# Kernel tuning notes

Hardware: AMD Instinct MI355X
Metric: run time of the kernel (lower is better)

## Reference

```python
import jax, jax.numpy as jnp
import numpy as np

N_PEGS = 32      # 33 holes, one empty at start
N_ACTIONS = 132  # 33 positions * 4 moves


def _constants():
    # English peg-solitaire board: 7x7 cross, 33 holes; hole 0 is the center (3,3).
    moves = np.array([[-1, 0], [1, 0], [0, -1], [0, 1]], dtype=np.int64)
    cells = [(i, j) for i in range(7) for j in range(7) if (2 <= i <= 4) or (2 <= j <= 4)]
    cells.remove((3, 3))
    grid = np.array([(3, 3)] + cells, dtype=np.int64)          # (33, 2)
    p2i = {tuple(p): k for k, p in enumerate(grid)}
    pos_ids = np.repeat(np.arange(33), 4)                      # (132,)
    move_ids = np.tile(np.arange(4), 33)                       # (132,)
    apos = grid[pos_ids]                                       # (132, 2)
    amov = moves[move_ids]
    midp = apos + amov
    tgtp = apos + 2 * amov
    mid_idx = np.array([p2i.get(tuple(p), 0) for p in midp], dtype=np.int64)
    tgt_idx = np.array([p2i.get(tuple(p), 0) for p in tgtp], dtype=np.int64)
    oob = np.array([(tuple(m) not in p2i) or (tuple(t) not in p2i)
                    for m, t in zip(midp, tgtp)], dtype=bool)  # (132,)
    return dict(
        action_pos_ids=jnp.asarray(pos_ids, dtype=jnp.int32),
        action_mid_indices=jnp.asarray(mid_idx, dtype=jnp.int32),
        action_target_indices=jnp.asarray(tgt_idx, dtype=jnp.int32),
        oob_mask=jnp.asarray(oob),
        i_indices=jnp.asarray(grid[:, 0], dtype=jnp.int32),
        j_indices=jnp.asarray(grid[:, 1], dtype=jnp.int32),
    )


def setup_inputs() -> dict:
    key = jax.random.key(0)
    n = 262144
    k1, k2, k3, k4 = jax.random.split(key, 4)
    pegs = (jax.random.uniform(k1, (n, 33)) > 0.5).astype(jnp.float32)
    n_pegs = jax.random.randint(k2, (n,), 2, 32).astype(jnp.int32)
    done = jnp.zeros((n,), dtype=bool)
    total_reward = jax.random.uniform(k3, (n,), dtype=jnp.float32)
    actions = jax.random.randint(k4, (n,), 0, N_ACTIONS).astype(jnp.int32)
    inp = {"pegs": pegs, "n_pegs": n_pegs, "done": done,
           "total_reward": total_reward, "actions": actions}
    inp.update(_constants())
    return inp


def _feasible(pegs, done, action_pos_ids, action_mid_indices,
              action_target_indices, oob_mask):
    # (n, 132) boolean feasible-action mask
    mask = ~oob_mask[None, :]
    no_peg = pegs == 0.0
    mask = mask & ~no_peg[:, action_pos_ids]          # source must have a peg
    mask = mask & (pegs[:, action_mid_indices] > 0)   # mid must have a peg
    mask = mask & (pegs[:, action_target_indices] == 0)  # target must be empty
    return mask & ~done[:, None]


def reference(pegs, n_pegs, done, total_reward, actions,
              action_pos_ids, action_mid_indices, action_target_indices,
              oob_mask, i_indices, j_indices):
    n = pegs.shape[0]
    env = jnp.arange(n)
    pos = action_pos_ids[actions]
    mid = action_mid_indices[actions]
    tgt = action_target_indices[actions]
    # execute the jump (same write order as torch: pos<-0, mid<-0, target<-1)
    pegs = pegs.at[env, pos].set(0.0).at[env, mid].set(0.0).at[env, tgt].set(1.0)
    n_pegs = n_pegs - 1
    rewards = jnp.where(n_pegs == 1, 1.0, 1.0 / (N_PEGS - 1)).astype(jnp.float32)
    done_win = n_pegs == 1
    feasible = _feasible(pegs, done, action_pos_ids, action_mid_indices,
                         action_target_indices, oob_mask)
    done_new = done_win | ~feasible.any(axis=1)
    total_reward = total_reward + rewards
    # state: (n, 7, 7, 3)
    ch0 = jnp.zeros((n, 7, 7), dtype=pegs.dtype).at[:, i_indices, j_indices].set(pegs)
    npf = n_pegs.astype(jnp.float32)
    peg_ratio = (npf - 1.0) / (N_PEGS - 1)
    removed_ratio = (N_PEGS - npf) / (N_PEGS - 1)
    states = jnp.stack([
        ch0,
        jnp.broadcast_to(peg_ratio[:, None, None], (n, 7, 7)),
        jnp.broadcast_to(removed_ratio[:, None, None], (n, 7, 7)),
    ], axis=-1)
    return rewards, states, done_new, pegs, n_pegs, total_reward
```

## Files before the change

### kernel.cpp

```cpp
#include <hip/hip_runtime.h>


#define NTH 256
#define WPB 4
#define EPW 64

typedef float f32x4 __attribute__((ext_vector_type(4)));

__device__ constexpr int C2B[33] = {
    24,  2,  3,  4,  9, 10, 11, 14, 15, 16, 17, 18, 19, 20,
    21, 22, 23, 25, 26, 27, 28, 29, 30, 31, 32, 33, 34,
    37, 38, 39, 44, 45, 46};

constexpr unsigned long long cross_mask() {
    unsigned long long b = 0;
    for (int i = 0; i < 7; ++i)
        for (int j = 0; j < 7; ++j)
            if ((i >= 2 && i <= 4) || (j >= 2 && j <= 4))
                b |= 1ull << (i * 7 + j);
    return b;
}
constexpr unsigned long long cols_le(int jmax) {
    unsigned long long b = 0;
    for (int i = 0; i < 7; ++i)
        for (int j = 0; j <= jmax; ++j) b |= 1ull << (i * 7 + j);
    return b;
}
constexpr unsigned long long cols_ge(int jmin) {
    unsigned long long b = 0;
    for (int i = 0; i < 7; ++i)
        for (int j = jmin; j < 7; ++j) b |= 1ull << (i * 7 + j);
    return b;
}
constexpr unsigned long long B_MASK = cross_mask();
constexpr unsigned long long C_LE4  = cols_le(4);
constexpr unsigned long long C_GE2  = cols_ge(2);

__device__ __forceinline__ void wave_lds_fence() {
    asm volatile("s_waitcnt lgkmcnt(0)" ::: "memory");
    __builtin_amdgcn_sched_barrier(0);
}

__global__ __launch_bounds__(NTH) void peg_step(
    const float* __restrict__ pegs_in,
    const int* __restrict__ n_pegs_in,
    const unsigned char* __restrict__ done_in,
    const float* __restrict__ tot_rew_in,
    const int* __restrict__ actions,
    const int* __restrict__ pos_ids,
    const int* __restrict__ mid_idx,
    const int* __restrict__ tgt_idx,
    const int* __restrict__ i_ind,
    const int* __restrict__ j_ind,
    float* __restrict__ out,
    int n)
{
    __shared__ __align__(16) float s_pegs[WPB][EPW * 33];
    __shared__ unsigned long long s_bb[WPB][EPW];
    __shared__ float s_r1[WPB][EPW], s_r2[WPB][EPW];

    const int t    = threadIdx.x;
    const int w    = t >> 6;
    const int lane = t & 63;
    const int ew0  = blockIdx.x * (WPB * EPW) + w * EPW;
    const int e    = ew0 + lane;

    {
        const f32x4* src = (const f32x4*)(pegs_in + (size_t)ew0 * 33);
        f32x4* dst = (f32x4*)s_pegs[w];
        #pragma unroll
        for (int i = lane; i < EPW * 33 / 4; i += 64) dst[i] = src[i];
    }

    const int a         = actions[e];
    const int np_new    = n_pegs_in[e] - 1;
    const bool done_old = (done_in[e] != 0);
    const float tot     = tot_rew_in[e];
    const int p = pos_ids[a], m = mid_idx[a], g = tgt_idx[a];
    const int bp = i_ind[p] * 7 + j_ind[p];
    const int bm = i_ind[m] * 7 + j_ind[m];
    const int bg = i_ind[g] * 7 + j_ind[g];

    const float rw  = (np_new == 1) ? 1.0f : (1.0f / 31.0f);
    const float npf = (float)np_new;
    out[e]                   = rw;
    out[(size_t)182 * n + e] = npf;
    out[(size_t)183 * n + e] = tot + rw;

    wave_lds_fence();

    float* row = s_pegs[w] + lane * 33;
    unsigned long long P = 0;
    #pragma unroll
    for (int c = 0; c < 33; ++c)
        P |= (unsigned long long)(row[c] != 0.0f) << C2B[c];

    row[p] = 0.0f;
    row[m] = 0.0f;
    row[g] = 1.0f;
    P &= ~(1ull << bp);
    P &= ~(1ull << bm);
    P |=  (1ull << bg);

    const unsigned long long E = ~P & B_MASK;
    const unsigned long long feas =
        (P & (P >> 1) & (E >> 2)  & C_LE4) |
        (P & (P << 1) & (E << 2)  & C_GE2) |
        (P & (P >> 7) & (E >> 14))         |
        (P & (P << 7) & (E << 14));

    const bool dn = (np_new == 1) | done_old | (feas == 0ull);
    out[(size_t)148 * n + e] = dn ? 1.0f : 0.0f;

    s_bb[w][lane] = P;
    s_r1[w][lane] = (npf - 1.0f)  * (1.0f / 31.0f);
    s_r2[w][lane] = (32.0f - npf) * (1.0f / 31.0f);

    wave_lds_fence();

    {
        const f32x4* src = (const f32x4*)s_pegs[w];
        f32x4* dst = (f32x4*)(out + (size_t)149 * n + (size_t)ew0 * 33);
        #pragma unroll
        for (int i = lane; i < EPW * 33 / 4; i += 64) dst[i] = src[i];
    }

    {
        f32x4* dst = (f32x4*)(out + (size_t)n + (size_t)ew0 * 147);
        const int total = EPW * 147 / 4;
        for (int q = lane; q < total; q += 64) {
            const int f4 = q * 4;
            int env = f4 / 147;
            int el  = f4 - env * 147;
            unsigned long long bb = s_bb[w][env];
            float r1 = s_r1[w][env], r2 = s_r2[w][env];
            f32x4 v;
            #pragma unroll
            for (int r = 0; r < 4; ++r) {
                if (el == 147) {
                    el = 0; ++env;
                    bb = s_bb[w][env]; r1 = s_r1[w][env]; r2 = s_r2[w][env];
                }
                const int rc = el / 3;
                const int ch = el - rc * 3;
                v[r] = (ch == 0) ? (float)((unsigned int)(bb >> rc) & 1u)
                                 : ((ch == 1) ? r1 : r2);
                ++el;
            }
            dst[q] = v;
        }
    }
}

extern "C" void kernel_launch(void* const* d_in, const int* in_sizes, int n_in,
                              void* d_out, int out_size, void* d_ws, size_t ws_size,
                              hipStream_t stream) {
    const float* pegs          = (const float*)d_in[0];
    const int* n_pegs          = (const int*)d_in[1];
    const unsigned char* done  = (const unsigned char*)d_in[2];
    const float* total_reward  = (const float*)d_in[3];
    const int* actions         = (const int*)d_in[4];
    const int* pos_ids         = (const int*)d_in[5];
    const int* mid_idx         = (const int*)d_in[6];
    const int* tgt_idx         = (const int*)d_in[7];
    const int* i_ind           = (const int*)d_in[9];
    const int* j_ind           = (const int*)d_in[10];
    float* out = (float*)d_out;

    int n = in_sizes[1];
    dim3 grid(n / (WPB * EPW)), block(NTH);
    hipLaunchKernelGGL(peg_step, grid, block, 0, stream,
                       pegs, n_pegs, done, total_reward, actions,
                       pos_ids, mid_idx, tgt_idx, i_ind, j_ind, out, n);
}
```

Before: 44.66 us.

## Pack peg rows into LDS bitmasks instead of staging float rows

New measurement: 44.83 us. About the same (+0.4%).

```diff
diff --git a/kernel.cpp b/kernel.cpp
--- a/kernel.cpp
+++ b/kernel.cpp
@@ -11,6 +11,8 @@
     24,  2,  3,  4,  9, 10, 11, 14, 15, 16, 17, 18, 19, 20,
     21, 22, 23, 25, 26, 27, 28, 29, 30, 31, 32, 33, 34,
     37, 38, 39, 44, 45, 46};
+
+constexpr unsigned long long MASK33 = (1ull << 33) - 1;
 
 constexpr unsigned long long cross_mask() {
     unsigned long long b = 0;
@@ -41,7 +43,7 @@
     __builtin_amdgcn_sched_barrier(0);
 }
 
-__global__ __launch_bounds__(NTH) void peg_step(
+__global__ __launch_bounds__(NTH, 6) void peg_step(
     const float* __restrict__ pegs_in,
     const int* __restrict__ n_pegs_in,
     const unsigned char* __restrict__ done_in,
@@ -50,12 +52,10 @@
     const int* __restrict__ pos_ids,
     const int* __restrict__ mid_idx,
     const int* __restrict__ tgt_idx,
-    const int* __restrict__ i_ind,
-    const int* __restrict__ j_ind,
     float* __restrict__ out,
     int n)
 {
-    __shared__ __align__(16) float s_pegs[WPB][EPW * 33];
+    __shared__ unsigned long long s_cm[WPB][EPW + 1];
     __shared__ unsigned long long s_bb[WPB][EPW];
     __shared__ float s_r1[WPB][EPW], s_r2[WPB][EPW];
 
@@ -65,21 +65,19 @@
     const int ew0  = blockIdx.x * (WPB * EPW) + w * EPW;
     const int e    = ew0 + lane;
 
-    {
-        const f32x4* src = (const f32x4*)(pegs_in + (size_t)ew0 * 33);
-        f32x4* dst = (f32x4*)s_pegs[w];
-        #pragma unroll
-        for (int i = lane; i < EPW * 33 / 4; i += 64) dst[i] = src[i];
-    }
+    s_cm[w][lane] = 0ull;
+
+    const f32x4* src = (const f32x4*)(pegs_in + (size_t)ew0 * 33);
+    f32x4 r[8], r8;
+    #pragma unroll
+    for (int k = 0; k < 8; ++k) r[k] = src[lane + 64 * k];
+    if (lane < 16) r8 = src[512 + lane];
 
     const int a         = actions[e];
     const int np_new    = n_pegs_in[e] - 1;
     const bool done_old = (done_in[e] != 0);
     const float tot     = tot_rew_in[e];
     const int p = pos_ids[a], m = mid_idx[a], g = tgt_idx[a];
-    const int bp = i_ind[p] * 7 + j_ind[p];
-    const int bm = i_ind[m] * 7 + j_ind[m];
-    const int bg = i_ind[g] * 7 + j_ind[g];
 
     const float rw  = (np_new == 1) ? 1.0f : (1.0f / 31.0f);
     const float npf = (float)np_new;
@@ -87,20 +85,46 @@
     out[(size_t)182 * n + e] = npf;
     out[(size_t)183 * n + e] = tot + rw;
 
+    {
+        unsigned long long* cm = s_cm[w];
+        #pragma unroll
+        for (int k = 0; k < 8; ++k) {
+            const int q   = lane + 64 * k;
+            const int f   = q * 4;
+            const int env = f / 33;
+            const int c   = f - env * 33;
+            const unsigned mm = (r[k][0] != 0.0f) | ((r[k][1] != 0.0f) << 1) |
+                                ((r[k][2] != 0.0f) << 2) | ((r[k][3] != 0.0f) << 3);
+            const unsigned long long full = (unsigned long long)mm << c;
+            atomicOr(&cm[env], full & MASK33);
+            const unsigned long long hi = full >> 33;
+            if (hi) atomicOr(&cm[env + 1], hi);
+        }
+        if (lane < 16) {
+            const int q   = 512 + lane;
+            const int f   = q * 4;
+            const int env = f / 33;
+            const int c   = f - env * 33;
+            const unsigned mm = (r8[0] != 0.0f) | ((r8[1] != 0.0f) << 1) |
+                                ((r8[2] != 0.0f) << 2) | ((r8[3] != 0.0f) << 3);
+            const unsigned long long full = (unsigned long long)mm << c;
+            atomicOr(&cm[env], full & MASK33);
+            const unsigned long long hi = full >> 33;
+            if (hi) atomicOr(&cm[env + 1], hi);
+        }
+    }
+
     wave_lds_fence();
 
-    float* row = s_pegs[w] + lane * 33;
+    unsigned long long cm = s_cm[w][lane];
+    cm &= ~(1ull << p);
+    cm &= ~(1ull << m);
+    cm |=  (1ull << g);
+
     unsigned long long P = 0;
     #pragma unroll
     for (int c = 0; c < 33; ++c)
-        P |= (unsigned long long)(row[c] != 0.0f) << C2B[c];
-
-    row[p] = 0.0f;
-    row[m] = 0.0f;
-    row[g] = 1.0f;
-    P &= ~(1ull << bp);
-    P &= ~(1ull << bm);
-    P |=  (1ull << bg);
+        P |= ((cm >> c) & 1ull) << C2B[c];
 
     const unsigned long long E = ~P & B_MASK;
     const unsigned long long feas =
@@ -112,6 +136,7 @@
     const bool dn = (np_new == 1) | done_old | (feas == 0ull);
     out[(size_t)148 * n + e] = dn ? 1.0f : 0.0f;
 
+    s_cm[w][lane] = cm;
     s_bb[w][lane] = P;
     s_r1[w][lane] = (npf - 1.0f)  * (1.0f / 31.0f);
     s_r2[w][lane] = (32.0f - npf) * (1.0f / 31.0f);
@@ -119,10 +144,23 @@
     wave_lds_fence();
 
     {
-        const f32x4* src = (const f32x4*)s_pegs[w];
         f32x4* dst = (f32x4*)(out + (size_t)149 * n + (size_t)ew0 * 33);
         #pragma unroll
-        for (int i = lane; i < EPW * 33 / 4; i += 64) dst[i] = src[i];
+        for (int k = 0; k < 9; ++k) {
+            const int q = lane + 64 * k;
+            if (k < 8 || lane < 16) {
+                const int f   = q * 4;
+                const int env = f / 33;
+                const int c   = f - env * 33;
+                const unsigned long long cat =
+                    s_cm[w][env] | (s_cm[w][env + 1] << 33);
+                f32x4 v;
+                #pragma unroll
+                for (int rr = 0; rr < 4; ++rr)
+                    v[rr] = (float)((unsigned int)(cat >> (c + rr)) & 1u);
+                dst[q] = v;
+            }
+        }
     }
 
     {
@@ -136,15 +174,15 @@
             float r1 = s_r1[w][env], r2 = s_r2[w][env];
             f32x4 v;
             #pragma unroll
-            for (int r = 0; r < 4; ++r) {
+            for (int rr = 0; rr < 4; ++rr) {
                 if (el == 147) {
                     el = 0; ++env;
                     bb = s_bb[w][env]; r1 = s_r1[w][env]; r2 = s_r2[w][env];
                 }
                 const int rc = el / 3;
                 const int ch = el - rc * 3;
-                v[r] = (ch == 0) ? (float)((unsigned int)(bb >> rc) & 1u)
-                                 : ((ch == 1) ? r1 : r2);
+                v[rr] = (ch == 0) ? (float)((unsigned int)(bb >> rc) & 1u)
+                                  : ((ch == 1) ? r1 : r2);
                 ++el;
             }
             dst[q] = v;
@@ -163,13 +201,11 @@
     const int* pos_ids         = (const int*)d_in[5];
     const int* mid_idx         = (const int*)d_in[6];
     const int* tgt_idx         = (const int*)d_in[7];
-    const int* i_ind           = (const int*)d_in[9];
-    const int* j_ind           = (const int*)d_in[10];
     float* out = (float*)d_out;
 
     int n = in_sizes[1];
     dim3 grid(n / (WPB * EPW)), block(NTH);
     hipLaunchKernelGGL(peg_step, grid, block, 0, stream,
                        pegs, n_pegs, done, total_reward, actions,
-                       pos_ids, mid_idx, tgt_idx, i_ind, j_ind, out, n);
-}
+                       pos_ids, mid_idx, tgt_idx, out, n);
+}
```
